# Kernel optimization log

Hardware: AMD Instinct MI355X
Metric: run time of the kernel (lower is better)

The kernel has to match this reference:

```python
import jax, jax.numpy as jnp
import numpy as np

N = 50000   # nodes
E = 800000  # edges
F = 256     # input features
H = 256     # hidden units
L = 128     # n_labels
EPS = 1e-5


def setup_inputs():
    key = jax.random.key(0)
    ks = jax.random.split(key, 17)
    s = 0.05
    return {
        "features": jax.random.normal(ks[0], (N, F), jnp.float32),
        "edge_vals": jax.random.uniform(ks[1], (E,), jnp.float32),
        "W1": jax.random.normal(ks[2], (F, H), jnp.float32) * s,
        "db1": jax.random.normal(ks[3], (H,), jnp.float32) * s,
        "b1": jax.random.normal(ks[4], (H,), jnp.float32) * s,
        "g1": jax.random.uniform(ks[5], (H,), jnp.float32, 0.5, 1.5),
        "be1": jax.random.normal(ks[6], (H,), jnp.float32) * s,
        "W2": jax.random.normal(ks[7], (H, H), jnp.float32) * s,
        "b2": jax.random.normal(ks[8], (H,), jnp.float32) * s,
        "g2": jax.random.uniform(ks[9], (H,), jnp.float32, 0.5, 1.5),
        "be2": jax.random.normal(ks[10], (H,), jnp.float32) * s,
        "Wf": jax.random.normal(ks[11], (H, L), jnp.float32) * s,
        "bf": jax.random.normal(ks[12], (L,), jnp.float32) * s,
        "edge_rows": jax.random.randint(ks[13], (E,), 0, N, jnp.int32),
        "edge_cols": jax.random.randint(ks[14], (E,), 0, N, jnp.int32),
        "idx": jax.random.randint(ks[15], (N // 2,), 0, N, jnp.int32),
    }


def _spmm(edge_vals, rows, cols, x):
    # out[i] = sum_{(i,j) in E} A[i,j] * x[j]  (COO sparse @ dense)
    return jax.ops.segment_sum(edge_vals[:, None] * x[cols], rows, num_segments=N)


def _bn(x, gamma, beta):
    # training-mode BatchNormalization: batch (population) stats over nodes
    m = jnp.mean(x, axis=0)
    v = jnp.var(x, axis=0)
    return (x - m) * jax.lax.rsqrt(v + EPS) * gamma + beta


def reference(features, edge_vals, W1, db1, b1, g1, be1, W2, b2, g2, be2, Wf, bf,
              edge_rows, edge_cols, idx):
    # layer 1 (Dense has bias only for l == 0)
    h = features @ W1 + db1
    h = _spmm(edge_vals, edge_rows, edge_cols, h) + b1
    h = jax.nn.relu(_bn(h, g1, be1))
    # layer 2 (no dense bias)
    h = h @ W2
    h = _spmm(edge_vals, edge_rows, edge_cols, h) + b2
    h = jax.nn.relu(_bn(h, g2, be2))
    # dropout = identity (deterministic baseline); final dense head
    out = h @ Wf + bf
    return out[idx]
```

## Files before the change

kernel.cpp:

```cpp
#include <hip/hip_runtime.h>
#include <stdint.h>

#define NN 50000
#define EE 800000
#define FF 256
#define HH 256
#define LL 128
#define SBLK 256

typedef __bf16 bf16x8 __attribute__((ext_vector_type(8)));
typedef float  f32x4  __attribute__((ext_vector_type(4)));

typedef __attribute__((address_space(1))) unsigned int uint_as1;
typedef __attribute__((address_space(3))) unsigned int uint_as3;

__device__ __forceinline__ unsigned short f2bf(float f) {
  union { float f; unsigned int u; } v; v.f = f;
  unsigned int u = v.u;
  u += 0x7FFFu + ((u >> 16) & 1u);
  return (unsigned short)(u >> 16);
}

__device__ __forceinline__ float bf2f(unsigned short u) {
  union { unsigned int u; float f; } v;
  v.u = ((unsigned int)u) << 16;
  return v.f;
}

__device__ __forceinline__ f32x4 bf4_to_f32(ushort4 u) {
  f32x4 r;
  r.x = bf2f(u.x); r.y = bf2f(u.y); r.z = bf2f(u.z); r.w = bf2f(u.w);
  return r;
}

__device__ __forceinline__ void gload_lds16(const void* g, void* l) {
  __builtin_amdgcn_global_load_lds((const uint_as1*)g, (uint_as3*)l, 16, 0, 0);
}

__global__ __launch_bounds__(256) void k_casts(const float* __restrict__ features,
                                               unsigned short* __restrict__ Xb,
                                               const float* __restrict__ W1,
                                               unsigned short* __restrict__ W1t,
                                               const float* __restrict__ W2,
                                               unsigned short* __restrict__ W2t,
                                               const float* __restrict__ Wf,
                                               unsigned short* __restrict__ Wft,
                                               int* __restrict__ cnt,
                                               int* __restrict__ statz) {
  __shared__ float tl[64 * 65];
  int b = blockIdx.x, t = threadIdx.x;
  if (b < 12500) {
    int i = b * 256 + t;
    f32x4 x = ((const f32x4*)features)[i];
    ushort4 o;
    o.x = f2bf(x.x); o.y = f2bf(x.y); o.z = f2bf(x.z); o.w = f2bf(x.w);
    ((ushort4*)Xb)[i] = o;
  } else if (b < 12540) {
    const float* in;
    unsigned short* out;
    int Nin, k0, n0;
    if (b < 12516) {
      in = W1; out = W1t; Nin = HH;
      int tt = b - 12500; k0 = (tt >> 2) * 64; n0 = (tt & 3) * 64;
    } else if (b < 12532) {
      in = W2; out = W2t; Nin = HH;
      int tt = b - 12516; k0 = (tt >> 2) * 64; n0 = (tt & 3) * 64;
    } else {
      in = Wf; out = Wft; Nin = LL;
      int tt = b - 12532; k0 = (tt >> 1) * 64; n0 = (tt & 1) * 64;
    }
#pragma unroll
    for (int j = 0; j < 16; ++j) {
      int idx = j * 256 + t;
      int r = idx >> 6, c = idx & 63;
      tl[r * 65 + c] = in[(size_t)(k0 + r) * Nin + n0 + c];
    }
    __syncthreads();
#pragma unroll
    for (int j = 0; j < 16; ++j) {
      int idx = j * 256 + t;
      int r = idx >> 6, c = idx & 63;
      out[(size_t)(n0 + r) * HH + k0 + c] = f2bf(tl[c * 65 + r]);
    }
  } else if (b < 12589) {
    int base = (b - 12540) * 1024 + t * 4;
    if (base + 3 < NN) {
      int4 z = {0, 0, 0, 0};
      *(int4*)(cnt + base) = z;
    } else {
      for (int j = 0; j < 4; ++j)
        if (base + j < NN) cnt[base + j] = 0;
    }
  } else {
    for (int i = t; i < 4 * HH + 64; i += 256) statz[i] = 0;
  }
}

__global__ __launch_bounds__(256) void k_hist(const int* __restrict__ rows,
                                              int* __restrict__ cnt, int E) {
  int i = blockIdx.x * 256 + threadIdx.x;
  if (i < E) atomicAdd(&cnt[rows[i]], 1);
}

__global__ __launch_bounds__(256) void k_alloc(const int* __restrict__ cnt,
                                               int* __restrict__ cursor,
                                               int* __restrict__ total, int n) {
  int i = blockIdx.x * 256 + threadIdx.x;
  int lane = threadIdx.x & 63;
  int c = (i < n) ? cnt[i] : 0;
  int incl = c;
#pragma unroll
  for (int off = 1; off < 64; off <<= 1) {
    int v = __shfl_up(incl, off, 64);
    if (lane >= off) incl += v;
  }
  int excl = incl - c;
  int wtot = __shfl(incl, 63, 64);
  int base = 0;
  if (lane == 0) base = atomicAdd(total, wtot);
  base = __shfl(base, 0, 64);
  if (i < n) cursor[i] = base + excl;
}

__global__ __launch_bounds__(256) void k_fill(const int* __restrict__ rows,
                                              const int* __restrict__ cols,
                                              const float* __restrict__ vals,
                                              int* __restrict__ cursor,
                                              unsigned int* __restrict__ csr, int E) {
  int i = blockIdx.x * 256 + threadIdx.x;
  if (i < E) {
    int p = atomicAdd(&cursor[rows[i]], 1);
    csr[p] = ((unsigned int)cols[i] << 16) | (unsigned int)f2bf(vals[i]);
  }
}

__global__ __launch_bounds__(256) void k_spmm(const unsigned short* __restrict__ X,
                                              const int* __restrict__ endp,
                                              const int* __restrict__ cnt,
                                              const unsigned int* __restrict__ csr,
                                              unsigned short* __restrict__ Y, int n) {
  int row = blockIdx.x * 4 + (threadIdx.x >> 6);
  int lane = threadIdx.x & 63;
  if (row >= n) return;
  int e = endp[row];
  int s = e - cnt[row];
  f32x4 a0 = {0.f, 0.f, 0.f, 0.f};
  f32x4 a1 = a0, a2 = a0, a3 = a0;
  int p = s;
  int e4 = s + ((e - s) & ~3);
  for (; p < e4; p += 4) {
    unsigned int c0 = csr[p + 0], c1 = csr[p + 1], c2 = csr[p + 2], c3 = csr[p + 3];
    ushort4 x0 = ((const ushort4*)(X + (size_t)(c0 >> 16) * HH))[lane];
    ushort4 x1 = ((const ushort4*)(X + (size_t)(c1 >> 16) * HH))[lane];
    ushort4 x2 = ((const ushort4*)(X + (size_t)(c2 >> 16) * HH))[lane];
    ushort4 x3 = ((const ushort4*)(X + (size_t)(c3 >> 16) * HH))[lane];
    a0 += bf2f((unsigned short)c0) * bf4_to_f32(x0);
    a1 += bf2f((unsigned short)c1) * bf4_to_f32(x1);
    a2 += bf2f((unsigned short)c2) * bf4_to_f32(x2);
    a3 += bf2f((unsigned short)c3) * bf4_to_f32(x3);
  }
  for (; p < e; ++p) {
    unsigned int c0 = csr[p];
    ushort4 x0 = ((const ushort4*)(X + (size_t)(c0 >> 16) * HH))[lane];
    a0 += bf2f((unsigned short)c0) * bf4_to_f32(x0);
  }
  f32x4 a = (a0 + a1) + (a2 + a3);
  ushort4 o;
  o.x = f2bf(a.x); o.y = f2bf(a.y); o.z = f2bf(a.z); o.w = f2bf(a.w);
  ((ushort4*)(Y + (size_t)row * HH))[lane] = o;
}

__global__ __launch_bounds__(256) void k_bnstats(const unsigned short* __restrict__ X,
                                                 float* __restrict__ part, int n) {
  __shared__ float red[4][64][9];
  const int w = threadIdx.x >> 6, l = threadIdx.x & 63;
  f32x4 s = {0.f, 0.f, 0.f, 0.f}, s2 = {0.f, 0.f, 0.f, 0.f};
  for (int r = blockIdx.x * 4 + w; r < n; r += gridDim.x * 4) {
    f32x4 v = bf4_to_f32(((const ushort4*)(X + (size_t)r * HH))[l]);
    s += v;
    s2 += v * v;
  }
#pragma unroll
  for (int j = 0; j < 4; ++j) { red[w][l][j] = s[j]; red[w][l][4 + j] = s2[j]; }
  __syncthreads();
  if (threadIdx.x < 64) {
    int ll = threadIdx.x;
#pragma unroll
    for (int j = 0; j < 8; ++j) {
      float v = red[0][ll][j] + red[1][ll][j] + red[2][ll][j] + red[3][ll][j];
      int c = ll * 4 + (j & 3);
      part[((j < 4) ? 0 : (SBLK * 256)) + blockIdx.x * 256 + c] = v;
    }
  }
}

__global__ __launch_bounds__(256) void k_bnred(const float* __restrict__ part,
                                               float* __restrict__ sums) {
  int c = threadIdx.x;
  int stat = blockIdx.x >> 3, chunk = blockIdx.x & 7;
  const float* p = part + stat * (SBLK * 256) + chunk * 32 * 256;
  float s0 = 0.f, s1 = 0.f, s2 = 0.f, s3 = 0.f;
  for (int b = 0; b < 32; b += 4) {
    s0 += p[(b + 0) * 256 + c];
    s1 += p[(b + 1) * 256 + c];
    s2 += p[(b + 2) * 256 + c];
    s3 += p[(b + 3) * 256 + c];
  }
  atomicAdd(&sums[stat * HH + c], (s0 + s1) + (s2 + s3));
}

__global__ __launch_bounds__(256) void k_bnrc(const unsigned short* __restrict__ X,
                                              const float* __restrict__ sums,
                                              const float* __restrict__ g,
                                              const float* __restrict__ be,
                                              unsigned short* __restrict__ out, int n4) {
  __shared__ float sc[HH], sh[HH];
  int t = threadIdx.x;
  {
    float inv = 1.f / (float)NN;
    float mean = sums[t] * inv;
    float var = sums[HH + t] * inv - mean * mean;
    float s = g[t] * rsqrtf(var + 1e-5f);
    sc[t] = s;
    sh[t] = be[t] - mean * s;
  }
  __syncthreads();
  for (int i = blockIdx.x * 256 + t; i < n4; i += gridDim.x * 256) {
    f32x4 x = bf4_to_f32(((const ushort4*)X)[i]);
    int c0 = (i * 4) & (HH - 1);
    ushort4 o;
    o.x = f2bf(fmaxf(x.x * sc[c0 + 0] + sh[c0 + 0], 0.f));
    o.y = f2bf(fmaxf(x.y * sc[c0 + 1] + sh[c0 + 1], 0.f));
    o.z = f2bf(fmaxf(x.z * sc[c0 + 2] + sh[c0 + 2], 0.f));
    o.w = f2bf(fmaxf(x.w * sc[c0 + 3] + sh[c0 + 3], 0.f));
    ((ushort4*)out)[i] = o;
  }
}

template <int OUTB>
__global__ __launch_bounds__(256, 2) void k_gemm(const unsigned short* __restrict__ A,
                                                 const unsigned short* __restrict__ Bt,
                                                 const float* __restrict__ bias,
                                                 void* __restrict__ Cv,
                                                 int M, int K, int Nn,
                                                 const int* __restrict__ gather) {
  __shared__ unsigned short lA[128 * 64];
  __shared__ unsigned short lB[128 * 64];
  const int tid = threadIdx.x;
  const int wave = tid >> 6, lane = tid & 63;
  const int m0 = blockIdx.x * 128, n0 = blockIdx.y * 128;
  const int wm = (wave >> 1) * 64, wn = (wave & 1) * 64;
  const int lhi = lane >> 4, llo = lane & 15;

  const int srow = lane >> 3;
  const int scol = (lane & 7) * 8;
  const unsigned short *pA[4], *pB[4];
#pragma unroll
  for (int j = 0; j < 4; ++j) {
    int base = (wave * 4 + j) * 8 + srow;
    int ar = m0 + base;
    ar = ar < M ? ar : 0;
    if (gather) ar = gather[ar];
    pA[j] = A + (size_t)ar * K + scol;
    pB[j] = Bt + (size_t)(n0 + base) * K + scol;
  }

  f32x4 zero = {0.f, 0.f, 0.f, 0.f};
  f32x4 acc[4][4];
#pragma unroll
  for (int i = 0; i < 4; ++i)
#pragma unroll
    for (int j = 0; j < 4; ++j) acc[i][j] = zero;

  for (int k0 = 0; k0 < K; k0 += 64) {
#pragma unroll
    for (int j = 0; j < 4; ++j) {
      gload_lds16(pA[j] + k0, lA + (wave * 4 + j) * 8 * 64);
      gload_lds16(pB[j] + k0, lB + (wave * 4 + j) * 8 * 64);
    }
    __syncthreads();
    bf16x8 af[2][4], bfv[2][4];
#pragma unroll
    for (int ks = 0; ks < 2; ++ks) {
#pragma unroll
      for (int mt = 0; mt < 4; ++mt)
        af[ks][mt] = *(const bf16x8*)(lA + (wm + mt * 16 + llo) * 64 + ks * 32 + lhi * 8);
#pragma unroll
      for (int nt = 0; nt < 4; ++nt)
        bfv[ks][nt] = *(const bf16x8*)(lB + (wn + nt * 16 + llo) * 64 + ks * 32 + lhi * 8);
    }
#pragma unroll
    for (int ks = 0; ks < 2; ++ks)
#pragma unroll
      for (int mt = 0; mt < 4; ++mt)
#pragma unroll
        for (int nt = 0; nt < 4; ++nt)
          acc[mt][nt] = __builtin_amdgcn_mfma_f32_16x16x32_bf16(af[ks][mt], bfv[ks][nt], acc[mt][nt], 0, 0, 0);
    __syncthreads();
  }

#pragma unroll
  for (int nt = 0; nt < 4; ++nt) {
    int cn = n0 + wn + nt * 16 + llo;
    float bv = bias ? bias[cn] : 0.f;
#pragma unroll
    for (int mt = 0; mt < 4; ++mt) {
      int cm0 = m0 + wm + mt * 16 + lhi * 4;
#pragma unroll
      for (int r = 0; r < 4; ++r) {
        int cm = cm0 + r;
        if (cm < M) {
          float v = acc[mt][nt][r] + bv;
          if (OUTB)
            ((unsigned short*)Cv)[(size_t)cm * Nn + cn] = f2bf(v);
          else
            ((float*)Cv)[(size_t)cm * Nn + cn] = v;
        }
      }
    }
  }
}

extern "C" void kernel_launch(void* const* d_in, const int* in_sizes, int n_in,
                              void* d_out, int out_size, void* d_ws, size_t ws_size,
                              hipStream_t stream) {
  const float* features = (const float*)d_in[0];
  const float* edge_vals = (const float*)d_in[1];
  const float* W1 = (const float*)d_in[2];
  const float* db1 = (const float*)d_in[3];
  const float* g1 = (const float*)d_in[5];
  const float* be1 = (const float*)d_in[6];
  const float* W2 = (const float*)d_in[7];
  const float* g2 = (const float*)d_in[9];
  const float* be2 = (const float*)d_in[10];
  const float* Wf = (const float*)d_in[11];
  const float* bfb = (const float*)d_in[12];
  const int* erows = (const int*)d_in[13];
  const int* ecols = (const int*)d_in[14];
  const int* idx = (const int*)d_in[15];
  const int M3 = in_sizes[15];
  (void)n_in; (void)out_size; (void)ws_size;

  char* ws = (char*)d_ws;
  size_t off = 0;
  auto alloc = [&](size_t bytes) -> void* {
    void* p = (void*)(ws + off);
    off += (bytes + 255) & ~(size_t)255;
    return p;
  };
  unsigned short* Xb = (unsigned short*)alloc((size_t)NN * HH * 2);
  unsigned short* Ab = (unsigned short*)alloc((size_t)NN * HH * 2);
  unsigned short* Yb = (unsigned short*)alloc((size_t)NN * HH * 2);
  unsigned short* W1t = (unsigned short*)alloc((size_t)FF * HH * 2);
  unsigned short* W2t = (unsigned short*)alloc((size_t)HH * HH * 2);
  unsigned short* Wft = (unsigned short*)alloc((size_t)HH * LL * 2);
  int* cursor = (int*)alloc((size_t)NN * 4);
  int* cnt = (int*)alloc((size_t)NN * 4);
  unsigned int* csr = (unsigned int*)alloc((size_t)EE * 4);
  float* part = (float*)alloc((size_t)2 * SBLK * 256 * 4);
  float* stats = (float*)alloc(4 * HH * 4 + 256);
  float* sums1 = stats;
  float* sums2 = stats + 2 * HH;
  int* total = (int*)(stats + 4 * HH);

  k_casts<<<12590, 256, 0, stream>>>(features, Xb, W1, W1t, W2, W2t, Wf, Wft,
                                     cnt, (int*)stats);

  k_hist<<<(EE + 255) / 256, 256, 0, stream>>>(erows, cnt, EE);
  k_alloc<<<(NN + 255) / 256, 256, 0, stream>>>(cnt, cursor, total, NN);
  k_fill<<<(EE + 255) / 256, 256, 0, stream>>>(erows, ecols, edge_vals, cursor, csr, EE);

  k_gemm<1><<<dim3((NN + 127) / 128, HH / 128), 256, 0, stream>>>(Xb, W1t, db1, Ab, NN, FF, HH, nullptr);
  k_spmm<<<(NN + 3) / 4, 256, 0, stream>>>(Ab, cursor, cnt, csr, Yb, NN);
  k_bnstats<<<SBLK, 256, 0, stream>>>(Yb, part, NN);
  k_bnred<<<16, 256, 0, stream>>>(part, sums1);
  k_bnrc<<<2048, 256, 0, stream>>>(Yb, sums1, g1, be1, Xb, NN * HH / 4);

  k_gemm<1><<<dim3((NN + 127) / 128, HH / 128), 256, 0, stream>>>(Xb, W2t, nullptr, Ab, NN, HH, HH, nullptr);
  k_spmm<<<(NN + 3) / 4, 256, 0, stream>>>(Ab, cursor, cnt, csr, Yb, NN);
  k_bnstats<<<SBLK, 256, 0, stream>>>(Yb, part, NN);
  k_bnred<<<16, 256, 0, stream>>>(part, sums2);
  k_bnrc<<<2048, 256, 0, stream>>>(Yb, sums2, g2, be2, Xb, NN * HH / 4);

  k_gemm<0><<<dim3((M3 + 127) / 128, LL / 128), 256, 0, stream>>>(Xb, Wft, bfb, d_out, M3, HH, LL, idx);
}
```

Measured before the change: 455.4 us.

## Normalize only gathered rows for head, widen fill, retune BN and GEMM occupancy

Result: no change. 463.8 us (+1.8%).

```diff
diff --git a/kernel.cpp b/kernel.cpp
--- a/kernel.cpp
+++ b/kernel.cpp
@@ -6,7 +6,7 @@
 #define FF 256
 #define HH 256
 #define LL 128
-#define SBLK 256
+#define SBLK 1024
 
 typedef __bf16 bf16x8 __attribute__((ext_vector_type(8)));
 typedef float  f32x4  __attribute__((ext_vector_type(4)));
@@ -127,8 +127,16 @@
                                               const float* __restrict__ vals,
                                               int* __restrict__ cursor,
                                               unsigned int* __restrict__ csr, int E) {
-  int i = blockIdx.x * 256 + threadIdx.x;
-  if (i < E) {
+  int i = (blockIdx.x * 256 + threadIdx.x) * 2;
+  if (i + 1 < E) {
+    int2 r2 = *(const int2*)(rows + i);
+    int2 c2 = *(const int2*)(cols + i);
+    float2 v2 = *(const float2*)(vals + i);
+    int p0 = atomicAdd(&cursor[r2.x], 1);
+    csr[p0] = ((unsigned int)c2.x << 16) | (unsigned int)f2bf(v2.x);
+    int p1 = atomicAdd(&cursor[r2.y], 1);
+    csr[p1] = ((unsigned int)c2.y << 16) | (unsigned int)f2bf(v2.y);
+  } else if (i < E) {
     int p = atomicAdd(&cursor[rows[i]], 1);
     csr[p] = ((unsigned int)cols[i] << 16) | (unsigned int)f2bf(vals[i]);
   }
@@ -198,9 +206,9 @@
                                                float* __restrict__ sums) {
   int c = threadIdx.x;
   int stat = blockIdx.x >> 3, chunk = blockIdx.x & 7;
-  const float* p = part + stat * (SBLK * 256) + chunk * 32 * 256;
+  const float* p = part + stat * (SBLK * 256) + chunk * 128 * 256;
   float s0 = 0.f, s1 = 0.f, s2 = 0.f, s3 = 0.f;
-  for (int b = 0; b < 32; b += 4) {
+  for (int b = 0; b < 128; b += 4) {
     s0 += p[(b + 0) * 256 + c];
     s1 += p[(b + 1) * 256 + c];
     s2 += p[(b + 2) * 256 + c];
@@ -237,13 +245,42 @@
   }
 }
 
+__global__ __launch_bounds__(256) void k_bnrc_pack(const unsigned short* __restrict__ X,
+                                                   const float* __restrict__ sums,
+                                                   const float* __restrict__ g,
+                                                   const float* __restrict__ be,
+                                                   const int* __restrict__ idx,
+                                                   unsigned short* __restrict__ out) {
+  __shared__ float sc[HH], sh[HH];
+  int t = threadIdx.x;
+  {
+    float inv = 1.f / (float)NN;
+    float mean = sums[t] * inv;
+    float var = sums[HH + t] * inv - mean * mean;
+    float s = g[t] * rsqrtf(var + 1e-5f);
+    sc[t] = s;
+    sh[t] = be[t] - mean * s;
+  }
+  __syncthreads();
+  int i = blockIdx.x * 256 + t;
+  int orow = i >> 6;
+  int c0 = (i & 63) * 4;
+  int irow = idx[orow];
+  f32x4 x = bf4_to_f32(*(const ushort4*)(X + (size_t)irow * HH + c0));
+  ushort4 o;
+  o.x = f2bf(fmaxf(x.x * sc[c0 + 0] + sh[c0 + 0], 0.f));
+  o.y = f2bf(fmaxf(x.y * sc[c0 + 1] + sh[c0 + 1], 0.f));
+  o.z = f2bf(fmaxf(x.z * sc[c0 + 2] + sh[c0 + 2], 0.f));
+  o.w = f2bf(fmaxf(x.w * sc[c0 + 3] + sh[c0 + 3], 0.f));
+  ((ushort4*)out)[i] = o;
+}
+
 template <int OUTB>
-__global__ __launch_bounds__(256, 2) void k_gemm(const unsigned short* __restrict__ A,
+__global__ __launch_bounds__(256, 3) void k_gemm(const unsigned short* __restrict__ A,
                                                  const unsigned short* __restrict__ Bt,
                                                  const float* __restrict__ bias,
                                                  void* __restrict__ Cv,
-                                                 int M, int K, int Nn,
-                                                 const int* __restrict__ gather) {
+                                                 int M, int K, int Nn) {
   __shared__ unsigned short lA[128 * 64];
   __shared__ unsigned short lB[128 * 64];
   const int tid = threadIdx.x;
@@ -260,7 +297,6 @@
     int base = (wave * 4 + j) * 8 + srow;
     int ar = m0 + base;
     ar = ar < M ? ar : 0;
-    if (gather) ar = gather[ar];
     pA[j] = A + (size_t)ar * K + scol;
     pB[j] = Bt + (size_t)(n0 + base) * K + scol;
   }
@@ -351,6 +387,7 @@
   unsigned short* Xb = (unsigned short*)alloc((size_t)NN * HH * 2);
   unsigned short* Ab = (unsigned short*)alloc((size_t)NN * HH * 2);
   unsigned short* Yb = (unsigned short*)alloc((size_t)NN * HH * 2);
+  unsigned short* Pb = (unsigned short*)alloc((size_t)25000 * HH * 2);
   unsigned short* W1t = (unsigned short*)alloc((size_t)FF * HH * 2);
   unsigned short* W2t = (unsigned short*)alloc((size_t)HH * HH * 2);
   unsigned short* Wft = (unsigned short*)alloc((size_t)HH * LL * 2);
@@ -368,19 +405,19 @@
 
   k_hist<<<(EE + 255) / 256, 256, 0, stream>>>(erows, cnt, EE);
   k_alloc<<<(NN + 255) / 256, 256, 0, stream>>>(cnt, cursor, total, NN);
-  k_fill<<<(EE + 255) / 256, 256, 0, stream>>>(erows, ecols, edge_vals, cursor, csr, EE);
-
-  k_gemm<1><<<dim3((NN + 127) / 128, HH / 128), 256, 0, stream>>>(Xb, W1t, db1, Ab, NN, FF, HH, nullptr);
+  k_fill<<<(EE / 2 + 255) / 256, 256, 0, stream>>>(erows, ecols, edge_vals, cursor, csr, EE);
+
+  k_gemm<1><<<dim3((NN + 127) / 128, HH / 128), 256, 0, stream>>>(Xb, W1t, db1, Ab, NN, FF, HH);
   k_spmm<<<(NN + 3) / 4, 256, 0, stream>>>(Ab, cursor, cnt, csr, Yb, NN);
   k_bnstats<<<SBLK, 256, 0, stream>>>(Yb, part, NN);
   k_bnred<<<16, 256, 0, stream>>>(part, sums1);
   k_bnrc<<<2048, 256, 0, stream>>>(Yb, sums1, g1, be1, Xb, NN * HH / 4);
 
-  k_gemm<1><<<dim3((NN + 127) / 128, HH / 128), 256, 0, stream>>>(Xb, W2t, nullptr, Ab, NN, HH, HH, nullptr);
+  k_gemm<1><<<dim3((NN + 127) / 128, HH / 128), 256, 0, stream>>>(Xb, W2t, nullptr, Ab, NN, HH, HH);
   k_spmm<<<(NN + 3) / 4, 256, 0, stream>>>(Ab, cursor, cnt, csr, Yb, NN);
   k_bnstats<<<SBLK, 256, 0, stream>>>(Yb, part, NN);
   k_bnred<<<16, 256, 0, stream>>>(part, sums2);
-  k_bnrc<<<2048, 256, 0, stream>>>(Yb, sums2, g2, be2, Xb, NN * HH / 4);
-
-  k_gemm<0><<<dim3((M3 + 127) / 128, LL / 128), 256, 0, stream>>>(Xb, Wft, bfb, d_out, M3, HH, LL, idx);
-}
+  k_bnrc_pack<<<(M3 * 64) / 256, 256, 0, stream>>>(Yb, sums2, g2, be2, idx, Pb);
+
+  k_gemm<0><<<dim3((M3 + 127) / 128, LL / 128), 256, 0, stream>>>(Pb, Wft, bfb, d_out, M3, HH, LL);
+}
```
